# Kernel optimization log

Measured on AMD Instinct MI355X. Metric: run time of the kernel, lower is better.

Reference implementation:

```python
import jax, jax.numpy as jnp
import numpy as np

B, C, H, W = 8, 512, 32, 32
NH, DH = 8, 64          # num_heads, head_dim (C = NH*DH)
GROUPS, EPS = 32, 1e-5


def group_norm(x, gamma, beta):
    b, c, h, w = x.shape
    xg = x.reshape(b, GROUPS, c // GROUPS, h, w)
    mu = xg.mean(axis=(2, 3, 4), keepdims=True)
    var = xg.var(axis=(2, 3, 4), keepdims=True)
    xn = ((xg - mu) * jax.lax.rsqrt(var + EPS)).reshape(b, c, h, w)
    return xn * gamma[:, None, None] + beta[:, None, None]


def conv1x1(x, w, b):
    # x: [B,C,H,W], w: [O,C], b: [O]
    return jnp.einsum('bchw,oc->bohw', x, w) + b[:, None, None]


def setup_inputs() -> dict:
    key = jax.random.key(0)
    ks = jax.random.split(key, 5)
    return {
        'x': jax.random.normal(ks[0], (B, C, H, W), jnp.float32),
        'norm_gamma': jnp.ones((C,), jnp.float32),
        'norm_beta': jnp.zeros((C,), jnp.float32),
        'qkv_w': jax.random.normal(ks[1], (3 * C, C), jnp.float32) * (1.0 / np.sqrt(C)),
        'qkv_b': jax.random.normal(ks[2], (3 * C,), jnp.float32) * 0.02,
        'proj_w': jax.random.normal(ks[3], (C, C), jnp.float32) * (1.0 / np.sqrt(C)),
        'proj_b': jax.random.normal(ks[4], (C,), jnp.float32) * 0.02,
    }


def reference(x, norm_gamma, norm_beta, qkv_w, qkv_b, proj_w, proj_b):
    scale = DH ** -0.5
    h = group_norm(x, norm_gamma, norm_beta)
    qkv = conv1x1(h, qkv_w, qkv_b)                       # [B,3C,H,W]
    qkv = qkv.reshape(B, 3, NH, DH, H * W)
    qkv = jnp.transpose(qkv, (1, 0, 2, 4, 3))            # [3,B,NH,HW,DH]
    q, k, v = qkv[0], qkv[1], qkv[2]
    attn = jnp.einsum('bhid,bhjd->bhij', q, k) * scale   # [B,NH,HW,HW]
    attn = jax.nn.softmax(attn, axis=-1)
    h = jnp.einsum('bhij,bhjd->bhid', attn, v)           # [B,NH,HW,DH]
    # faithful to torch: direct row-major reshape [B,NH,HW,DH] -> [B,C,H,W]
    h = h.reshape(B, C, H, W)
    h = conv1x1(h, proj_w, proj_b)
    return x + h
```

## Files before the change

### kernel.cpp

```cpp
#include <hip/hip_runtime.h>


typedef float  f32x4  __attribute__((ext_vector_type(4)));
typedef __bf16 bf16x8 __attribute__((ext_vector_type(8)));
typedef __bf16 bf16x4 __attribute__((ext_vector_type(4)));

#define MFMA(a, b, c) __builtin_amdgcn_mfma_f32_16x16x32_bf16(a, b, c, 0, 0, 0)

__device__ __forceinline__ void async16(const __bf16* g, __bf16* l) {
  __builtin_amdgcn_global_load_lds((const __attribute__((address_space(1))) void*)g,
                                   (__attribute__((address_space(3))) void*)l, 16, 0, 0);
}

__device__ __forceinline__ int chk(int n, int c) {
  return ((((n >> 6) * 16 + (c >> 5)) * 4 + ((c >> 3) & 3)) * 512) + (n & 63) * 8 + (c & 7);
}

__global__ __launch_bounds__(256) void cvt2_k(const float* __restrict__ qw, __bf16* __restrict__ dq,
                                              const float* __restrict__ pw, __bf16* __restrict__ dp) {
  int i = (blockIdx.x * 256 + threadIdx.x) * 4;
  const float* src = (i < 786432) ? qw : pw;
  __bf16* dst = (i < 786432) ? dq : dp;
  int j = (i < 786432) ? i : (i - 786432);
  int m = j >> 9, k = j & 511;
  float4 v = *(const float4*)(src + j);
  bf16x4 o;
  o[0] = (__bf16)v.x; o[1] = (__bf16)v.y; o[2] = (__bf16)v.z; o[3] = (__bf16)v.w;
  *(bf16x4*)(dst + chk(m, k)) = o;
}

__global__ __launch_bounds__(256) void groupnorm_k(const float* __restrict__ x,
                                                   const float* __restrict__ gamma,
                                                   const float* __restrict__ beta,
                                                   __bf16* __restrict__ Hout) {
  __shared__ __bf16 xs[16 * 1032];
  __shared__ float  red[8];
  __shared__ float  ga[16], be[16], stat[2];
  const int tid = threadIdx.x;
  const int w = tid >> 6, l = tid & 63;
  const int bg = blockIdx.x, b = bg >> 5, g = bg & 31, c0 = g * 16;
  const float* xg = x + b * 524288 + c0 * 1024;

  float sum = 0.f, sq = 0.f;
#pragma unroll
  for (int p = 0; p < 16; p++) {
    int idx = p * 1024 + tid * 4;
    float4 v = *(const float4*)(xg + idx);
    int c = idx >> 10, s = idx & 1023;
    bf16x4 o;
    o[0] = (__bf16)v.x; o[1] = (__bf16)v.y; o[2] = (__bf16)v.z; o[3] = (__bf16)v.w;
    *(bf16x4*)(&xs[c * 1032 + s]) = o;
    sum += v.x + v.y + v.z + v.w;
    sq  += v.x * v.x + v.y * v.y + v.z * v.z + v.w * v.w;
  }
#pragma unroll
  for (int o = 32; o > 0; o >>= 1) { sum += __shfl_down(sum, o); sq += __shfl_down(sq, o); }
  if (l == 0) { red[w * 2] = sum; red[w * 2 + 1] = sq; }
  __syncthreads();
  if (tid == 0) {
    float S = red[0] + red[2] + red[4] + red[6];
    float Q = red[1] + red[3] + red[5] + red[7];
    float mean = S * (1.f / 16384.f);
    float var  = Q * (1.f / 16384.f) - mean * mean;
    stat[0] = mean; stat[1] = rsqrtf(var + 1e-5f);
  }
  if (tid < 16) { ga[tid] = gamma[c0 + tid]; be[tid] = beta[c0 + tid]; }
  __syncthreads();
  const float mean = stat[0], rstd = stat[1];
#pragma unroll
  for (int p = 0; p < 4; p++) {
    int s = p * 256 + tid;
    int n = b * 1024 + s;
    bf16x8 o0, o1;
#pragma unroll
    for (int c = 0; c < 8; c++) {
      float f = (float)xs[c * 1032 + s];
      o0[c] = (__bf16)((f - mean) * rstd * ga[c] + be[c]);
    }
#pragma unroll
    for (int c = 8; c < 16; c++) {
      float f = (float)xs[c * 1032 + s];
      o1[c - 8] = (__bf16)((f - mean) * rstd * ga[c] + be[c]);
    }
    *(bf16x8*)(Hout + chk(n, c0)) = o0;
    *(bf16x8*)(Hout + chk(n, c0 + 8)) = o1;
  }
}

__global__ __launch_bounds__(256) void gemm_qkv_k(const __bf16* __restrict__ W,
                                                  const float* __restrict__ bias,
                                                  const __bf16* __restrict__ H,
                                                  __bf16* __restrict__ qbuf,
                                                  __bf16* __restrict__ kbuf,
                                                  __bf16* __restrict__ vbuf) {
  __shared__ union {
    struct { __bf16 a[2][4096]; __bf16 b[2][4096]; } ab;
    __bf16 cs[128 * 136];
  } lds;
  const int tid = threadIdx.x;
  const int w = tid >> 6, l = tid & 63, quad = l >> 4, li = l & 15;
  const int wr = w >> 1, wc = w & 1;
  const int mblk = blockIdx.x >> 6, nblk = blockIdx.x & 63;
  const int m0 = mblk * 128, n0 = nblk * 128;

  f32x4 acc[4][4];
#pragma unroll
  for (int i = 0; i < 4; i++)
#pragma unroll
    for (int j = 0; j < 4; j++) acc[i][j] = f32x4{0.f, 0.f, 0.f, 0.f};

  const __bf16* Ag = W + (((m0 >> 6) * 16) * 4 + w) * 512 + l * 8;
  const __bf16* Bg = H + (((n0 >> 6) * 16) * 4 + w) * 512 + l * 8;
  const int halfA = 16 * 4 * 512;

  async16(Ag,         &lds.ab.a[0][w * 1024]);
  async16(Ag + halfA, &lds.ab.a[0][w * 1024 + 512]);
  async16(Bg,         &lds.ab.b[0][w * 1024]);
  async16(Bg + halfA, &lds.ab.b[0][w * 1024 + 512]);

#pragma unroll 1
  for (int kt = 0; kt < 16; kt++) {
    int cur = kt & 1, nxt = cur ^ 1;
    __syncthreads();
    if (kt < 15) {
      int ko = (kt + 1) * 2048;
      async16(Ag + ko,          &lds.ab.a[nxt][w * 1024]);
      async16(Ag + halfA + ko,  &lds.ab.a[nxt][w * 1024 + 512]);
      async16(Bg + ko,          &lds.ab.b[nxt][w * 1024]);
      async16(Bg + halfA + ko,  &lds.ab.b[nxt][w * 1024 + 512]);
    }
    bf16x8 af[4], bfr[4];
#pragma unroll
    for (int i = 0; i < 4; i++)
      af[i] = *(const bf16x8*)(&lds.ab.a[cur][quad * 1024 + (wr * 64 + i * 16 + li) * 8]);
#pragma unroll
    for (int i = 0; i < 4; i++)
      bfr[i] = *(const bf16x8*)(&lds.ab.b[cur][quad * 1024 + (wc * 64 + i * 16 + li) * 8]);
#pragma unroll
    for (int i = 0; i < 4; i++)
#pragma unroll
      for (int j = 0; j < 4; j++) acc[i][j] = MFMA(af[i], bfr[j], acc[i][j]);
  }

  const int t = m0 >> 9;
  const int cbase = m0 & 511;
  __syncthreads();
#pragma unroll
  for (int mi = 0; mi < 4; mi++) {
    int olocal = wr * 64 + mi * 16 + quad * 4;
    float bs[4];
#pragma unroll
    for (int r = 0; r < 4; r++) bs[r] = bias[m0 + olocal + r];
#pragma unroll
    for (int ni = 0; ni < 4; ni++) {
      int nlocal = wc * 64 + ni * 16 + li;
      bf16x4 pk;
#pragma unroll
      for (int r = 0; r < 4; r++) {
        float f = acc[mi][ni][r] + bs[r];
        if (t == 0) f *= 0.180336880f;
        pk[r] = (__bf16)f;
      }
      *(bf16x4*)(&lds.cs[nlocal * 136 + olocal]) = pk;
    }
  }
  __syncthreads();
  if (t < 2) {
    __bf16* dst = (t == 0) ? qbuf : kbuf;
    const int bb = n0 >> 10, s0 = n0 & 1023, nh0 = cbase >> 6;
#pragma unroll
    for (int p = 0; p < 8; p++) {
      int idx = p * 256 + tid;
      int oc = idx & 15, nloc = idx >> 4;
      uint4 val = *(const uint4*)(&lds.cs[nloc * 136 + oc * 8]);
      int bh = bb * 8 + nh0 + (oc >> 3);
      int s = s0 + nloc, d0 = (oc & 7) * 8;
      *(uint4*)(dst + (((bh * 16 + (s >> 6)) * 8 + (d0 >> 3)) * 64 + (s & 63)) * 8) = val;
    }
  } else {
#pragma unroll
    for (int p = 0; p < 8; p++) {
      int idx = p * 256 + tid;
      int o = idx & 127, ng = idx >> 7;
      bf16x8 vv;
#pragma unroll
      for (int jj = 0; jj < 8; jj++) vv[jj] = lds.cs[(ng * 8 + jj) * 136 + o];
      *(bf16x8*)(vbuf + (cbase + o) * 8192 + n0 + ng * 8) = vv;
    }
  }
}

__global__ __launch_bounds__(256) void attn_k(const __bf16* __restrict__ qb,
                                              const __bf16* __restrict__ kb,
                                              const __bf16* __restrict__ vb,
                                              __bf16* __restrict__ pin) {
  __shared__ __bf16 KC[2][4096];
  __shared__ __bf16 VC[2][4096];
  __shared__ union { __bf16 q[8192]; __bf16 p[128 * 72]; } PQ;
  const int tid = threadIdx.x;
  const int w = tid >> 6, l = tid & 63, quad = l >> 4, li = l & 15;
  const int bh = blockIdx.x >> 3, qt = blockIdx.x & 7;
  const int b = bh >> 3, nh = bh & 7;
  const __bf16* Qg = qb + bh * 16 * 4096;
  const __bf16* Kg = kb + bh * 16 * 4096;
  const __bf16* Vg = vb + (nh * 64) * 8192 + b * 1024;

#pragma unroll
  for (int p = 0; p < 4; p++) {
    int e = w + 4 * p, tb = e >> 3, ch = e & 7;
    async16(Qg + (((qt * 2 + tb) * 8 + ch) * 64) * 8 + l * 8, &PQ.q[ch * 1024 + tb * 512 + l * 8]);
  }
#pragma unroll
  for (int p = 0; p < 2; p++) {
    int ch = w + 4 * p;
    async16(Kg + ((ch) * 64) * 8 + l * 8,       &KC[0][ch * 512 + l * 8]);
    async16(Vg + l * 8192 + ch * 8,             &VC[0][ch * 512 + l * 8]);
  }
  __syncthreads();
  bf16x8 qf[2][2];
#pragma unroll
  for (int it = 0; it < 2; it++)
#pragma unroll
    for (int ks = 0; ks < 2; ks++)
      qf[it][ks] = *(const bf16x8*)(&PQ.q[(ks * 4 + quad) * 1024 + (w * 32 + it * 16 + li) * 8]);
  __syncthreads();

  float mrun[2] = {-1e30f, -1e30f}, lrun[2] = {0.f, 0.f};
  f32x4 oacc[2][4];
#pragma unroll
  for (int it = 0; it < 2; it++)
#pragma unroll
    for (int dt = 0; dt < 4; dt++) oacc[it][dt] = f32x4{0.f, 0.f, 0.f, 0.f};

#pragma unroll 1
  for (int kv = 0; kv < 16; kv++) {
    int cur = kv & 1, nxt = cur ^ 1;
    if (kv < 15) {
#pragma unroll
      for (int p = 0; p < 2; p++) {
        int ch = w + 4 * p;
        async16(Kg + (((kv + 1) * 8 + ch) * 64) * 8 + l * 8, &KC[nxt][ch * 512 + l * 8]);
        async16(Vg + l * 8192 + (kv + 1) * 64 + ch * 8,      &VC[nxt][ch * 512 + l * 8]);
      }
    }

    f32x4 st[2][4];
#pragma unroll
    for (int it = 0; it < 2; it++)
#pragma unroll
      for (int jt = 0; jt < 4; jt++) st[it][jt] = f32x4{0.f, 0.f, 0.f, 0.f};
#pragma unroll
    for (int ks = 0; ks < 2; ks++)
#pragma unroll
      for (int jt = 0; jt < 4; jt++) {
        bf16x8 kf = *(const bf16x8*)(&KC[cur][(ks * 4 + quad) * 512 + (jt * 16 + li) * 8]);
        st[0][jt] = MFMA(kf, qf[0][ks], st[0][jt]);
        st[1][jt] = MFMA(kf, qf[1][ks], st[1][jt]);
      }

#pragma unroll
    for (int it = 0; it < 2; it++) {
      float mt = -1e30f;
#pragma unroll
      for (int jt = 0; jt < 4; jt++)
#pragma unroll
        for (int r = 0; r < 4; r++) mt = fmaxf(mt, st[it][jt][r]);
      mt = fmaxf(mt, __shfl_xor(mt, 16));
      mt = fmaxf(mt, __shfl_xor(mt, 32));
      float mnew = fmaxf(mrun[it], mt);
      float alpha = __builtin_amdgcn_exp2f(mrun[it] - mnew);
      mrun[it] = mnew;
      float ls0 = 0.f, ls1 = 0.f;
#pragma unroll
      for (int jt = 0; jt < 4; jt++) {
        f32x4 v = st[it][jt];
        bf16x4 pk;
        float p0 = __builtin_amdgcn_exp2f(v[0] - mnew);
        float p1 = __builtin_amdgcn_exp2f(v[1] - mnew);
        float p2 = __builtin_amdgcn_exp2f(v[2] - mnew);
        float p3 = __builtin_amdgcn_exp2f(v[3] - mnew);
        ls0 += p0 + p1; ls1 += p2 + p3;
        pk[0] = (__bf16)p0; pk[1] = (__bf16)p1; pk[2] = (__bf16)p2; pk[3] = (__bf16)p3;
        *(bf16x4*)(&PQ.p[(w * 32 + it * 16 + li) * 72 + jt * 16 + quad * 4]) = pk;
      }
      float ls = ls0 + ls1;
      ls += __shfl_xor(ls, 16);
      ls += __shfl_xor(ls, 32);
      lrun[it] = lrun[it] * alpha + ls;
#pragma unroll
      for (int r = 0; r < 4; r++) {
        float ab = __shfl(alpha, quad * 4 + r);
#pragma unroll
        for (int dt = 0; dt < 4; dt++) oacc[it][dt][r] *= ab;
      }
    }

#pragma unroll
    for (int ks2 = 0; ks2 < 2; ks2++) {
      bf16x8 pf0 = *(const bf16x8*)(&PQ.p[(w * 32 + li) * 72 + ks2 * 32 + quad * 8]);
      bf16x8 pf1 = *(const bf16x8*)(&PQ.p[(w * 32 + 16 + li) * 72 + ks2 * 32 + quad * 8]);
#pragma unroll
      for (int dt = 0; dt < 4; dt++) {
        bf16x8 vf = *(const bf16x8*)(&VC[cur][(ks2 * 4 + quad) * 512 + (dt * 16 + li) * 8]);
        oacc[0][dt] = MFMA(pf0, vf, oacc[0][dt]);
        oacc[1][dt] = MFMA(pf1, vf, oacc[1][dt]);
      }
    }
    __syncthreads();
  }

  const float inv0 = 1.f / lrun[0], inv1 = 1.f / lrun[1];
#pragma unroll
  for (int it = 0; it < 2; it++) {
    float invv = it ? inv1 : inv0;
#pragma unroll
    for (int r = 0; r < 4; r++) {
      float ib = __shfl(invv, quad * 4 + r);
      int row = w * 32 + it * 16 + quad * 4 + r;
#pragma unroll
      for (int dt = 0; dt < 4; dt++)
        PQ.p[row * 72 + dt * 16 + li] = (__bf16)(oacc[it][dt][r] * ib);
    }
  }
  __syncthreads();
#pragma unroll
  for (int p = 0; p < 4; p++) {
    int idx = p * 256 + tid, d = idx & 63, ilo = idx >> 6;
    bf16x8 vv;
#pragma unroll
    for (int ihi = 0; ihi < 8; ihi++) vv[ihi] = PQ.p[(ihi * 16 + ilo) * 72 + d];
    int off = ((((b * 16 + ilo) * 16 + nh * 2 + (qt >> 2)) * 4 + (qt & 3)) * 64 + d) * 8;
    *(bf16x8*)(pin + off) = vv;
  }
}

__global__ __launch_bounds__(256) void gemm_proj_k(const __bf16* __restrict__ W,
                                                   const float* __restrict__ bias,
                                                   const __bf16* __restrict__ P,
                                                   const float* __restrict__ x,
                                                   float* __restrict__ out) {
  __shared__ __bf16 AL[2][2048];
  __shared__ __bf16 BL[2][4096];
  const int tid = threadIdx.x;
  const int w = tid >> 6, l = tid & 63, quad = l >> 4, li = l & 15;
  const int wr = w >> 1, wc = w & 1;
  const int mblk = blockIdx.x >> 6, nblk = blockIdx.x & 63;
  const int m0 = mblk * 64, n0 = nblk * 128;

  f32x4 acc[2][4];
#pragma unroll
  for (int i = 0; i < 2; i++)
#pragma unroll
    for (int j = 0; j < 4; j++) acc[i][j] = f32x4{0.f, 0.f, 0.f, 0.f};

  const __bf16* Ag = W + ((mblk * 16) * 4 + w) * 512 + l * 8;
  const __bf16* Bg = P + (((n0 >> 6) * 16) * 4 + w) * 512 + l * 8;
  const int halfB = 16 * 4 * 512;

  async16(Ag,         &AL[0][w * 512]);
  async16(Bg,         &BL[0][w * 1024]);
  async16(Bg + halfB, &BL[0][w * 1024 + 512]);

#pragma unroll 1
  for (int kt = 0; kt < 16; kt++) {
    int cur = kt & 1, nxt = cur ^ 1;
    __syncthreads();
    if (kt < 15) {
      int ko = (kt + 1) * 2048;
      async16(Ag + ko,          &AL[nxt][w * 512]);
      async16(Bg + ko,          &BL[nxt][w * 1024]);
      async16(Bg + halfB + ko,  &BL[nxt][w * 1024 + 512]);
    }
    bf16x8 af[2], bfr[4];
#pragma unroll
    for (int i = 0; i < 2; i++)
      af[i] = *(const bf16x8*)(&AL[cur][quad * 512 + (wr * 32 + i * 16 + li) * 8]);
#pragma unroll
    for (int j = 0; j < 4; j++)
      bfr[j] = *(const bf16x8*)(&BL[cur][quad * 1024 + (wc * 64 + j * 16 + li) * 8]);
#pragma unroll
    for (int i = 0; i < 2; i++)
#pragma unroll
      for (int j = 0; j < 4; j++) acc[i][j] = MFMA(af[i], bfr[j], acc[i][j]);
  }

  const int bb = n0 >> 10;
#pragma unroll
  for (int mi = 0; mi < 2; mi++) {
    int o = m0 + wr * 32 + mi * 16 + quad * 4;
    float bs[4];
#pragma unroll
    for (int r = 0; r < 4; r++) bs[r] = bias[o + r];
#pragma unroll
    for (int ni = 0; ni < 4; ni++) {
      int n = n0 + wc * 64 + ni * 16 + li;
      int s = n & 1023;
#pragma unroll
      for (int r = 0; r < 4; r++) {
        int a = (bb * 512 + o + r) * 1024 + s;
        out[a] = acc[mi][ni][r] + bs[r] + x[a];
      }
    }
  }
}

extern "C" void kernel_launch(void* const* d_in, const int* in_sizes, int n_in,
                              void* d_out, int out_size, void* d_ws, size_t ws_size,
                              hipStream_t stream) {
  const float* x      = (const float*)d_in[0];
  const float* gamma  = (const float*)d_in[1];
  const float* beta   = (const float*)d_in[2];
  const float* qkv_w  = (const float*)d_in[3];
  const float* qkv_b  = (const float*)d_in[4];
  const float* proj_w = (const float*)d_in[5];
  const float* proj_b = (const float*)d_in[6];

  __bf16* ws   = (__bf16*)d_ws;
  __bf16* H    = ws;
  __bf16* qbuf = ws + 4194304;
  __bf16* kbuf = ws + 8388608;
  __bf16* vbuf = ws + 12582912;
  __bf16* wq   = ws + 16777216;
  __bf16* wp   = ws + 17563648;

  cvt2_k<<<1024, 256, 0, stream>>>(qkv_w, wq, proj_w, wp);
  groupnorm_k<<<256, 256, 0, stream>>>(x, gamma, beta, H);
  gemm_qkv_k<<<768, 256, 0, stream>>>(wq, qkv_b, H, qbuf, kbuf, vbuf);
  attn_k<<<512, 256, 0, stream>>>(qbuf, kbuf, vbuf, H);
  gemm_proj_k<<<512, 256, 0, stream>>>(wp, proj_b, H, x, (float*)d_out);
}
```

Measured before the change: 157.8 us.

## Retile attention to 64-query blocks with pre-chunked V and simpler output layout

```diff
diff --git a/kernel.cpp b/kernel.cpp
--- a/kernel.cpp
+++ b/kernel.cpp
@@ -29,12 +29,12 @@
   *(bf16x4*)(dst + chk(m, k)) = o;
 }
 
-__global__ __launch_bounds__(256) void groupnorm_k(const float* __restrict__ x,
+__global__ __launch_bounds__(512) void groupnorm_k(const float* __restrict__ x,
                                                    const float* __restrict__ gamma,
                                                    const float* __restrict__ beta,
                                                    __bf16* __restrict__ Hout) {
   __shared__ __bf16 xs[16 * 1032];
-  __shared__ float  red[8];
+  __shared__ float  red[16];
   __shared__ float  ga[16], be[16], stat[2];
   const int tid = threadIdx.x;
   const int w = tid >> 6, l = tid & 63;
@@ -43,8 +43,8 @@
 
   float sum = 0.f, sq = 0.f;
 #pragma unroll
-  for (int p = 0; p < 16; p++) {
-    int idx = p * 1024 + tid * 4;
+  for (int p = 0; p < 8; p++) {
+    int idx = p * 2048 + tid * 4;
     float4 v = *(const float4*)(xg + idx);
     int c = idx >> 10, s = idx & 1023;
     bf16x4 o;
@@ -58,8 +58,9 @@
   if (l == 0) { red[w * 2] = sum; red[w * 2 + 1] = sq; }
   __syncthreads();
   if (tid == 0) {
-    float S = red[0] + red[2] + red[4] + red[6];
-    float Q = red[1] + red[3] + red[5] + red[7];
+    float S = 0.f, Q = 0.f;
+#pragma unroll
+    for (int i = 0; i < 8; i++) { S += red[i * 2]; Q += red[i * 2 + 1]; }
     float mean = S * (1.f / 16384.f);
     float var  = Q * (1.f / 16384.f) - mean * mean;
     stat[0] = mean; stat[1] = rsqrtf(var + 1e-5f);
@@ -68,8 +69,8 @@
   __syncthreads();
   const float mean = stat[0], rstd = stat[1];
 #pragma unroll
-  for (int p = 0; p < 4; p++) {
-    int s = p * 256 + tid;
+  for (int p = 0; p < 2; p++) {
+    int s = p * 512 + tid;
     int n = b * 1024 + s;
     bf16x8 o0, o1;
 #pragma unroll
@@ -92,7 +93,7 @@
                                                   const __bf16* __restrict__ H,
                                                   __bf16* __restrict__ qbuf,
                                                   __bf16* __restrict__ kbuf,
-                                                  __bf16* __restrict__ vbuf) {
+                                                  __bf16* __restrict__ vt) {
   __shared__ union {
     struct { __bf16 a[2][4096]; __bf16 b[2][4096]; } ab;
     __bf16 cs[128 * 136];
@@ -165,9 +166,10 @@
     }
   }
   __syncthreads();
+  const int bb = n0 >> 10, s0 = n0 & 1023;
   if (t < 2) {
     __bf16* dst = (t == 0) ? qbuf : kbuf;
-    const int bb = n0 >> 10, s0 = n0 & 1023, nh0 = cbase >> 6;
+    const int nh0 = cbase >> 6;
 #pragma unroll
     for (int p = 0; p < 8; p++) {
       int idx = p * 256 + tid;
@@ -182,55 +184,52 @@
     for (int p = 0; p < 8; p++) {
       int idx = p * 256 + tid;
       int o = idx & 127, ng = idx >> 7;
+      int c = cbase + o, nh2 = c >> 6, d = c & 63;
+      int bh = bb * 8 + nh2;
+      int j0 = s0 + ng * 8;
       bf16x8 vv;
 #pragma unroll
       for (int jj = 0; jj < 8; jj++) vv[jj] = lds.cs[(ng * 8 + jj) * 136 + o];
-      *(bf16x8*)(vbuf + (cbase + o) * 8192 + n0 + ng * 8) = vv;
+      *(bf16x8*)(vt + (((bh * 16 + (j0 >> 6)) * 8 + ((j0 >> 3) & 7)) * 64 + d) * 8) = vv;
     }
   }
 }
 
 __global__ __launch_bounds__(256) void attn_k(const __bf16* __restrict__ qb,
                                               const __bf16* __restrict__ kb,
-                                              const __bf16* __restrict__ vb,
+                                              const __bf16* __restrict__ vt,
                                               __bf16* __restrict__ pin) {
   __shared__ __bf16 KC[2][4096];
   __shared__ __bf16 VC[2][4096];
-  __shared__ union { __bf16 q[8192]; __bf16 p[128 * 72]; } PQ;
+  __shared__ union { __bf16 q[4096]; __bf16 p[4096]; __bf16 o[4096]; } PQ;
   const int tid = threadIdx.x;
   const int w = tid >> 6, l = tid & 63, quad = l >> 4, li = l & 15;
-  const int bh = blockIdx.x >> 3, qt = blockIdx.x & 7;
+  const int x = blockIdx.x;
+  const int qt = (x >> 3) & 15;
+  const int bh = (x & 7) | ((x >> 7) << 3);
   const int b = bh >> 3, nh = bh & 7;
-  const __bf16* Qg = qb + bh * 16 * 4096;
-  const __bf16* Kg = kb + bh * 16 * 4096;
-  const __bf16* Vg = vb + (nh * 64) * 8192 + b * 1024;
-
-#pragma unroll
-  for (int p = 0; p < 4; p++) {
-    int e = w + 4 * p, tb = e >> 3, ch = e & 7;
-    async16(Qg + (((qt * 2 + tb) * 8 + ch) * 64) * 8 + l * 8, &PQ.q[ch * 1024 + tb * 512 + l * 8]);
-  }
+  const __bf16* Qg = qb + bh * 65536;
+  const __bf16* Kg = kb + bh * 65536;
+  const __bf16* Vg = vt + bh * 65536;
+
 #pragma unroll
   for (int p = 0; p < 2; p++) {
     int ch = w + 4 * p;
-    async16(Kg + ((ch) * 64) * 8 + l * 8,       &KC[0][ch * 512 + l * 8]);
-    async16(Vg + l * 8192 + ch * 8,             &VC[0][ch * 512 + l * 8]);
-  }
-  __syncthreads();
-  bf16x8 qf[2][2];
-#pragma unroll
-  for (int it = 0; it < 2; it++)
-#pragma unroll
-    for (int ks = 0; ks < 2; ks++)
-      qf[it][ks] = *(const bf16x8*)(&PQ.q[(ks * 4 + quad) * 1024 + (w * 32 + it * 16 + li) * 8]);
-  __syncthreads();
-
-  float mrun[2] = {-1e30f, -1e30f}, lrun[2] = {0.f, 0.f};
-  f32x4 oacc[2][4];
-#pragma unroll
-  for (int it = 0; it < 2; it++)
-#pragma unroll
-    for (int dt = 0; dt < 4; dt++) oacc[it][dt] = f32x4{0.f, 0.f, 0.f, 0.f};
+    async16(Qg + ((qt * 8 + ch) * 64) * 8 + l * 8, &PQ.q[ch * 512 + l * 8]);
+    async16(Kg + (ch * 64) * 8 + l * 8,            &KC[0][ch * 512 + l * 8]);
+    async16(Vg + (ch * 64) * 8 + l * 8,            &VC[0][ch * 512 + l * 8]);
+  }
+  __syncthreads();
+  bf16x8 qf[2];
+#pragma unroll
+  for (int ks = 0; ks < 2; ks++)
+    qf[ks] = *(const bf16x8*)(&PQ.q[(ks * 4 + quad) * 512 + (w * 16 + li) * 8]);
+  __syncthreads();
+
+  float mrun = -1e30f, lrun = 0.f;
+  f32x4 oacc[4];
+#pragma unroll
+  for (int dt = 0; dt < 4; dt++) oacc[dt] = f32x4{0.f, 0.f, 0.f, 0.f};
 
 #pragma unroll 1
   for (int kv = 0; kv < 16; kv++) {
@@ -240,97 +239,82 @@
       for (int p = 0; p < 2; p++) {
         int ch = w + 4 * p;
         async16(Kg + (((kv + 1) * 8 + ch) * 64) * 8 + l * 8, &KC[nxt][ch * 512 + l * 8]);
-        async16(Vg + l * 8192 + (kv + 1) * 64 + ch * 8,      &VC[nxt][ch * 512 + l * 8]);
+        async16(Vg + (((kv + 1) * 8 + ch) * 64) * 8 + l * 8, &VC[nxt][ch * 512 + l * 8]);
       }
     }
 
-    f32x4 st[2][4];
-#pragma unroll
-    for (int it = 0; it < 2; it++)
-#pragma unroll
-      for (int jt = 0; jt < 4; jt++) st[it][jt] = f32x4{0.f, 0.f, 0.f, 0.f};
+    f32x4 st[4];
+#pragma unroll
+    for (int jt = 0; jt < 4; jt++) st[jt] = f32x4{0.f, 0.f, 0.f, 0.f};
 #pragma unroll
     for (int ks = 0; ks < 2; ks++)
 #pragma unroll
       for (int jt = 0; jt < 4; jt++) {
         bf16x8 kf = *(const bf16x8*)(&KC[cur][(ks * 4 + quad) * 512 + (jt * 16 + li) * 8]);
-        st[0][jt] = MFMA(kf, qf[0][ks], st[0][jt]);
-        st[1][jt] = MFMA(kf, qf[1][ks], st[1][jt]);
+        st[jt] = MFMA(kf, qf[ks], st[jt]);
       }
 
-#pragma unroll
-    for (int it = 0; it < 2; it++) {
-      float mt = -1e30f;
-#pragma unroll
-      for (int jt = 0; jt < 4; jt++)
-#pragma unroll
-        for (int r = 0; r < 4; r++) mt = fmaxf(mt, st[it][jt][r]);
-      mt = fmaxf(mt, __shfl_xor(mt, 16));
-      mt = fmaxf(mt, __shfl_xor(mt, 32));
-      float mnew = fmaxf(mrun[it], mt);
-      float alpha = __builtin_amdgcn_exp2f(mrun[it] - mnew);
-      mrun[it] = mnew;
-      float ls0 = 0.f, ls1 = 0.f;
-#pragma unroll
-      for (int jt = 0; jt < 4; jt++) {
-        f32x4 v = st[it][jt];
-        bf16x4 pk;
-        float p0 = __builtin_amdgcn_exp2f(v[0] - mnew);
-        float p1 = __builtin_amdgcn_exp2f(v[1] - mnew);
-        float p2 = __builtin_amdgcn_exp2f(v[2] - mnew);
-        float p3 = __builtin_amdgcn_exp2f(v[3] - mnew);
-        ls0 += p0 + p1; ls1 += p2 + p3;
-        pk[0] = (__bf16)p0; pk[1] = (__bf16)p1; pk[2] = (__bf16)p2; pk[3] = (__bf16)p3;
-        *(bf16x4*)(&PQ.p[(w * 32 + it * 16 + li) * 72 + jt * 16 + quad * 4]) = pk;
-      }
-      float ls = ls0 + ls1;
-      ls += __shfl_xor(ls, 16);
-      ls += __shfl_xor(ls, 32);
-      lrun[it] = lrun[it] * alpha + ls;
-#pragma unroll
-      for (int r = 0; r < 4; r++) {
-        float ab = __shfl(alpha, quad * 4 + r);
-#pragma unroll
-        for (int dt = 0; dt < 4; dt++) oacc[it][dt][r] *= ab;
-      }
+    float mt = -1e30f;
+#pragma unroll
+    for (int jt = 0; jt < 4; jt++)
+#pragma unroll
+      for (int r = 0; r < 4; r++) mt = fmaxf(mt, st[jt][r]);
+    mt = fmaxf(mt, __shfl_xor(mt, 16));
+    mt = fmaxf(mt, __shfl_xor(mt, 32));
+    float mnew = fmaxf(mrun, mt);
+    float alpha = __builtin_amdgcn_exp2f(mrun - mnew);
+    mrun = mnew;
+    float ls0 = 0.f, ls1 = 0.f;
+#pragma unroll
+    for (int jt = 0; jt < 4; jt++) {
+      f32x4 v = st[jt];
+      bf16x4 pk;
+      float p0 = __builtin_amdgcn_exp2f(v[0] - mnew);
+      float p1 = __builtin_amdgcn_exp2f(v[1] - mnew);
+      float p2 = __builtin_amdgcn_exp2f(v[2] - mnew);
+      float p3 = __builtin_amdgcn_exp2f(v[3] - mnew);
+      ls0 += p0 + p1; ls1 += p2 + p3;
+      pk[0] = (__bf16)p0; pk[1] = (__bf16)p1; pk[2] = (__bf16)p2; pk[3] = (__bf16)p3;
+      *(bf16x4*)(&PQ.p[w * 1024 + (jt * 2 + (quad >> 1)) * 128 + li * 8 + (quad & 1) * 4]) = pk;
+    }
+    float ls = ls0 + ls1;
+    ls += __shfl_xor(ls, 16);
+    ls += __shfl_xor(ls, 32);
+    lrun = lrun * alpha + ls;
+#pragma unroll
+    for (int r = 0; r < 4; r++) {
+      float ab = __shfl(alpha, quad * 4 + r);
+#pragma unroll
+      for (int dt = 0; dt < 4; dt++) oacc[dt][r] *= ab;
     }
 
 #pragma unroll
     for (int ks2 = 0; ks2 < 2; ks2++) {
-      bf16x8 pf0 = *(const bf16x8*)(&PQ.p[(w * 32 + li) * 72 + ks2 * 32 + quad * 8]);
-      bf16x8 pf1 = *(const bf16x8*)(&PQ.p[(w * 32 + 16 + li) * 72 + ks2 * 32 + quad * 8]);
+      bf16x8 pf = *(const bf16x8*)(&PQ.p[w * 1024 + (ks2 * 4 + quad) * 128 + li * 8]);
 #pragma unroll
       for (int dt = 0; dt < 4; dt++) {
         bf16x8 vf = *(const bf16x8*)(&VC[cur][(ks2 * 4 + quad) * 512 + (dt * 16 + li) * 8]);
-        oacc[0][dt] = MFMA(pf0, vf, oacc[0][dt]);
-        oacc[1][dt] = MFMA(pf1, vf, oacc[1][dt]);
+        oacc[dt] = MFMA(pf, vf, oacc[dt]);
       }
     }
     __syncthreads();
   }
 
-  const float inv0 = 1.f / lrun[0], inv1 = 1.f / lrun[1];
-#pragma unroll
-  for (int it = 0; it < 2; it++) {
-    float invv = it ? inv1 : inv0;
-#pragma unroll
-    for (int r = 0; r < 4; r++) {
-      float ib = __shfl(invv, quad * 4 + r);
-      int row = w * 32 + it * 16 + quad * 4 + r;
-#pragma unroll
-      for (int dt = 0; dt < 4; dt++)
-        PQ.p[row * 72 + dt * 16 + li] = (__bf16)(oacc[it][dt][r] * ib);
-    }
-  }
-  __syncthreads();
+  const float inv = 1.f / lrun;
+#pragma unroll
+  for (int r = 0; r < 4; r++) {
+    float ib = __shfl(inv, quad * 4 + r);
+#pragma unroll
+    for (int dt = 0; dt < 4; dt++)
+      PQ.o[((quad * 4 + r) * 64 + dt * 16 + li) * 4 + w] = (__bf16)(oacc[dt][r] * ib);
+  }
+  __syncthreads();
+  __bf16* Pg = pin + (nh * 8 + (qt >> 1)) * 65536 + (qt & 1) * 4 + b * 8192;
 #pragma unroll
   for (int p = 0; p < 4; p++) {
-    int idx = p * 256 + tid, d = idx & 63, ilo = idx >> 6;
-    bf16x8 vv;
-#pragma unroll
-    for (int ihi = 0; ihi < 8; ihi++) vv[ihi] = PQ.p[(ihi * 16 + ilo) * 72 + d];
-    int off = ((((b * 16 + ilo) * 16 + nh * 2 + (qt >> 2)) * 4 + (qt & 3)) * 64 + d) * 8;
-    *(bf16x8*)(pin + off) = vv;
+    int n = p * 256 + tid;
+    bf16x4 ov = *(const bf16x4*)(&PQ.o[n * 4]);
+    *(bf16x4*)(Pg + n * 8) = ov;
   }
 }
 
@@ -354,22 +338,22 @@
     for (int j = 0; j < 4; j++) acc[i][j] = f32x4{0.f, 0.f, 0.f, 0.f};
 
   const __bf16* Ag = W + ((mblk * 16) * 4 + w) * 512 + l * 8;
-  const __bf16* Bg = P + (((n0 >> 6) * 16) * 4 + w) * 512 + l * 8;
-  const int halfB = 16 * 4 * 512;
-
-  async16(Ag,         &AL[0][w * 512]);
-  async16(Bg,         &BL[0][w * 1024]);
-  async16(Bg + halfB, &BL[0][w * 1024 + 512]);
+  const __bf16* Bg = P + w * 65536 + (n0 + l) * 8;
+
+  async16(Ag,       &AL[0][w * 512]);
+  async16(Bg,       &BL[0][w * 1024]);
+  async16(Bg + 512, &BL[0][w * 1024 + 512]);
 
 #pragma unroll 1
   for (int kt = 0; kt < 16; kt++) {
     int cur = kt & 1, nxt = cur ^ 1;
     __syncthreads();
     if (kt < 15) {
-      int ko = (kt + 1) * 2048;
-      async16(Ag + ko,          &AL[nxt][w * 512]);
-      async16(Bg + ko,          &BL[nxt][w * 1024]);
-      async16(Bg + halfB + ko,  &BL[nxt][w * 1024 + 512]);
+      int koA = (kt + 1) * 2048;
+      int koB = (kt + 1) * 262144;
+      async16(Ag + koA,       &AL[nxt][w * 512]);
+      async16(Bg + koB,       &BL[nxt][w * 1024]);
+      async16(Bg + koB + 512, &BL[nxt][w * 1024 + 512]);
     }
     bf16x8 af[2], bfr[4];
 #pragma unroll
@@ -419,13 +403,13 @@
   __bf16* H    = ws;
   __bf16* qbuf = ws + 4194304;
   __bf16* kbuf = ws + 8388608;
-  __bf16* vbuf = ws + 12582912;
+  __bf16* vt   = ws + 12582912;
   __bf16* wq   = ws + 16777216;
   __bf16* wp   = ws + 17563648;
 
   cvt2_k<<<1024, 256, 0, stream>>>(qkv_w, wq, proj_w, wp);
-  groupnorm_k<<<256, 256, 0, stream>>>(x, gamma, beta, H);
-  gemm_qkv_k<<<768, 256, 0, stream>>>(wq, qkv_b, H, qbuf, kbuf, vbuf);
-  attn_k<<<512, 256, 0, stream>>>(qbuf, kbuf, vbuf, H);
+  groupnorm_k<<<256, 512, 0, stream>>>(x, gamma, beta, H);
+  gemm_qkv_k<<<768, 256, 0, stream>>>(wq, qkv_b, H, qbuf, kbuf, vt);
+  attn_k<<<1024, 256, 0, stream>>>(qbuf, kbuf, vt, H);
   gemm_proj_k<<<512, 256, 0, stream>>>(wp, proj_b, H, x, (float*)d_out);
 }
```

New measurement: 152.6 us. 1.03x faster.
